# Performance work log

Measured on AMD Instinct MI355X. Metric: run time of the kernel, lower is better.

The kernel has to match this reference:

```python
import jax, jax.numpy as jnp
import numpy as np

N, H, E, C, V, K = 4096, 256, 128, 32, 64, 20


def setup_inputs() -> dict:
    key = jax.random.key(0)
    ks = jax.random.split(key, 16)
    f = lambda k, s: jax.random.normal(k, s, dtype=jnp.float32)
    return {
        "vec": f(ks[0], (N, H)),
        "inp": f(ks[1], (N, E)),
        "h_prev": f(ks[2], (N, H)),
        "c_prev": f(ks[3], (N, H)),
        "Wlin": f(ks[4], (C, V, H)) * 0.05,
        "blin": f(ks[5], (C, V)) * 0.05,
        "Wec": f(ks[6], (2, H)) * 0.05,
        "bec": f(ks[7], (2,)) * 0.05,
        "Wrel": f(ks[8], (5, H)) * 0.05,
        "brel": f(ks[9], (5,)) * 0.05,
        "W_ih": f(ks[10], (K, 4 * H, E)) * 0.05,
        "b_ih": f(ks[11], (K, 4 * H)) * 0.05,
        "W_hh": f(ks[12], (K, 4 * H, H)) * 0.05,
        "b_hh": f(ks[13], (K, 4 * H)) * 0.05,
        "category": jax.random.randint(ks[14], (N,), 0, C, dtype=jnp.int32),
        "cell_id": jax.random.randint(ks[15], (N,), 0, K, dtype=jnp.int32),
        "true_idx": jax.random.randint(jax.random.fold_in(key, 100), (N,), 0, V, dtype=jnp.int32),
        "ec_idx": jax.random.randint(jax.random.fold_in(key, 101), (N,), 0, 2, dtype=jnp.int32),
        "rel_idx": jax.random.randint(jax.random.fold_in(key, 102), (N,), 0, 5, dtype=jnp.int32),
    }


def _ce(logits, targets):
    # per-row cross entropy (same math as nn.CrossEntropyLoss per example)
    logp = jax.nn.log_softmax(logits, axis=-1)
    return -jnp.take_along_axis(logp, targets[:, None], axis=-1)[:, 0]


def reference(vec, inp, h_prev, c_prev, Wlin, blin, Wec, bec, Wrel, brel,
              W_ih, b_ih, W_hh, b_hh, category, cell_id, true_idx, ec_idx, rel_idx):
    # --- get_log_odds: per-category tiny linear head, selected by category ---
    logits_all = jnp.einsum('nh,cvh->ncv', vec, Wlin) + blin          # [N,C,V]
    logits = jnp.take_along_axis(logits_all, category[:, None, None].astype(jnp.int32), axis=1)[:, 0]  # [N,V]
    logits_ec = vec @ Wec.T + bec                                      # [N,2]
    logits_rel = vec @ Wrel.T + brel                                   # [N,5]

    # --- calculate_loss: CE over valid children + ec + rel ---
    losses = _ce(logits, true_idx) + _ce(logits_ec, ec_idx) + _ce(logits_rel, rel_idx)  # [N]

    # --- get_next: per-child-index LSTMCell, selected by cell_id ---
    gates_all = (jnp.einsum('ne,kge->nkg', inp, W_ih)
                 + jnp.einsum('nh,kgh->nkg', h_prev, W_hh)
                 + b_ih + b_hh)                                        # [N,K,4H]
    gates = jnp.take_along_axis(gates_all, cell_id[:, None, None].astype(jnp.int32), axis=1)[:, 0]  # [N,4H]
    i, f, g, o = jnp.split(gates, 4, axis=-1)                          # torch LSTMCell gate order i,f,g,o
    c_next = jax.nn.sigmoid(f) * c_prev + jax.nn.sigmoid(i) * jnp.tanh(g)
    h_next = jax.nn.sigmoid(o) * jnp.tanh(c_next)

    # pack: [N, 1 + 2H] = loss | h_next | c_next
    return jnp.concatenate([losses[:, None], h_next, c_next], axis=-1)
```

## Files before the change

kernel.cpp:

```cpp
#include <hip/hip_runtime.h>
#include <hip/hip_bf16.h>
#include <math.h>

#define Nn 4096
#define Hdim 256
#define Edim 128
#define Cdim 32
#define Vdim 64
#define Kdim 20
#define G4H 1024
#define OUTS 513

#define SK 512
#define SC 256
#define RK_OFF 64
#define RC_OFF (RK_OFF + Kdim * SK)
#define NLI 18496
#define NSI 18497
#define ITL 18498
#define ITS (ITL + 640)

#define LSTM_REGION 592
#define LOSS_REGION 320
#define GRID (LSTM_REGION + LOSS_REGION)

typedef short bf16x8 __attribute__((ext_vector_type(8)));
typedef float f32x4 __attribute__((ext_vector_type(4)));

__device__ __forceinline__ float sigmoidf_(float x) { return 1.0f / (1.0f + expf(-x)); }

__device__ __forceinline__ bf16x8 cvt8(float4 f0, float4 f1) {
    bf16x8 r;
    __hip_bfloat16 h;
    h = __float2bfloat16(f0.x); r[0] = *(short*)&h;
    h = __float2bfloat16(f0.y); r[1] = *(short*)&h;
    h = __float2bfloat16(f0.z); r[2] = *(short*)&h;
    h = __float2bfloat16(f0.w); r[3] = *(short*)&h;
    h = __float2bfloat16(f1.x); r[4] = *(short*)&h;
    h = __float2bfloat16(f1.y); r[5] = *(short*)&h;
    h = __float2bfloat16(f1.z); r[6] = *(short*)&h;
    h = __float2bfloat16(f1.w); r[7] = *(short*)&h;
    return r;
}

__device__ __forceinline__ void gl_lds16(const float* g, void* l) {
    __builtin_amdgcn_global_load_lds((const __attribute__((address_space(1))) void*)g,
                                     (__attribute__((address_space(3))) void*)l, 16, 0, 0);
}

__device__ __forceinline__ int swz(int r) { return ((r & 3) << 1) | ((r >> 2) & 1); }

__global__ __launch_bounds__(1024) void k_bucket(const int* __restrict__ cell_id,
                                                 const int* __restrict__ category,
                                                 int* __restrict__ ws) {
    __shared__ int cnt[32];
    __shared__ int off[33];
    int t = threadIdx.x;
    if (t < 32) cnt[t] = 0;
    __syncthreads();
    int i0 = t * 4;
    if (blockIdx.x == 0) {
        int4 v = ((const int4*)cell_id)[t];
        int r;
        r = atomicAdd(&cnt[v.x], 1); if (r < SK) ws[RK_OFF + v.x * SK + r] = i0 + 0;
        r = atomicAdd(&cnt[v.y], 1); if (r < SK) ws[RK_OFF + v.y * SK + r] = i0 + 1;
        r = atomicAdd(&cnt[v.z], 1); if (r < SK) ws[RK_OFF + v.z * SK + r] = i0 + 2;
        r = atomicAdd(&cnt[v.w], 1); if (r < SK) ws[RK_OFF + v.w * SK + r] = i0 + 3;
        __syncthreads();
        if (t == 0) {
            int a = 0;
            for (int kk = 0; kk < Kdim; kk++) { off[kk] = a; a += (min(cnt[kk], SK) + 31) >> 5; }
            ws[NLI] = a * 4;
        }
        __syncthreads();
        if (t < Kdim) {
            int ns = (min(cnt[t], SK) + 31) >> 5;
            int base = off[t];
            for (int s = 0; s < ns; s++)
                for (int hq = 0; hq < 4; hq++)
                    ws[ITL + (base + s) * 4 + hq] = t | (s << 8) | (hq << 16);
        }
        if (t < 32) ws[t] = min(cnt[t], SK);
    } else {
        int4 v = ((const int4*)category)[t];
        int r;
        r = atomicAdd(&cnt[v.x], 1); if (r < SC) ws[RC_OFF + v.x * SC + r] = i0 + 0;
        r = atomicAdd(&cnt[v.y], 1); if (r < SC) ws[RC_OFF + v.y * SC + r] = i0 + 1;
        r = atomicAdd(&cnt[v.z], 1); if (r < SC) ws[RC_OFF + v.z * SC + r] = i0 + 2;
        r = atomicAdd(&cnt[v.w], 1); if (r < SC) ws[RC_OFF + v.w * SC + r] = i0 + 3;
        __syncthreads();
        if (t == 0) {
            int a = 0;
            for (int cc = 0; cc < Cdim; cc++) { off[cc] = a; a += (min(cnt[cc], SC) + 15) >> 4; }
            ws[NSI] = a;
        }
        __syncthreads();
        if (t < Cdim) {
            int ns = (min(cnt[t], SC) + 15) >> 4;
            int base = off[t];
            for (int s = 0; s < ns; s++)
                ws[ITS + base + s] = t | (s << 8);
        }
        if (t < 32) ws[32 + t] = min(cnt[t], SC);
    }
}

__global__ __launch_bounds__(256, 4) void k_main(
    const float* __restrict__ vec, const float* __restrict__ inp,
    const float* __restrict__ h_prev, const float* __restrict__ c_prev,
    const float* __restrict__ Wlin, const float* __restrict__ blin,
    const float* __restrict__ Wec, const float* __restrict__ bec,
    const float* __restrict__ Wrel, const float* __restrict__ brel,
    const float* __restrict__ W_ih, const float* __restrict__ b_ih,
    const float* __restrict__ W_hh, const float* __restrict__ b_hh,
    const int* __restrict__ true_idx, const int* __restrict__ ec_idx, const int* __restrict__ rel_idx,
    const int* __restrict__ ws,
    float* __restrict__ out)
{
    __shared__ __align__(16) char smem[36864];

    int b = blockIdx.x, t = threadIdx.x;
    int w = t >> 6, l = t & 63;
    int l15 = l & 15, quad = l >> 4;
    int lrow8 = l >> 3, lslot = l & 7;
    int p0 = (quad * 2) ^ swz(l15);

    if (b < LSTM_REGION) {
        if (b >= ws[NLI]) return;
        int item = ws[ITL + b];
        int k = item & 255, s = (item >> 8) & 255, hq = item >> 16;
        int cntk = ws[k];
        int rcount = min(32, cntk - s * 32);
        int reg_row = ws[RK_OFF + k * SK + s * 32 + min(l & 31, rcount - 1)];

        float* Wb = (float*)smem;
        float* Xb = (float*)(smem + 32768);
        const float* Wih_k = W_ih + (size_t)k * G4H * Edim;
        const float* Whh_k = W_hh + (size_t)k * G4H * Hdim;

        int xr = w * 8 + lrow8;
        int xrow = __shfl(reg_row, xr);
        int xg = lslot ^ swz(xr);

        int h = hq * 64 + w * 16 + l15;
        float bs[4];
        #pragma unroll
        for (int g = 0; g < 4; g++)
            bs[g] = b_ih[(size_t)k * G4H + g * Hdim + h] + b_hh[(size_t)k * G4H + g * Hdim + h];
        float cp[2][4];
        #pragma unroll
        for (int m = 0; m < 2; m++)
            #pragma unroll
            for (int reg = 0; reg < 4; reg++) {
                int r = m * 16 + quad * 4 + reg;
                int row = __shfl(reg_row, r);
                cp[m][reg] = c_prev[(size_t)row * Hdim + h];
            }

        f32x4 acc[2][4];
        #pragma unroll
        for (int m = 0; m < 2; m++)
            #pragma unroll
            for (int g = 0; g < 4; g++)
                acc[m][g] = (f32x4){0.f, 0.f, 0.f, 0.f};

        for (int st = 0; st < 12; st++) {
            int k0 = st * 32;
            const float* Wsrc; int stride, ko;
            if (k0 < Edim) { Wsrc = Wih_k; stride = Edim; ko = k0; }
            else           { Wsrc = Whh_k; stride = Hdim; ko = k0 - Edim; }
            __syncthreads();
            #pragma unroll
            for (int j = 0; j < 8; j++) {
                int r = w * 64 + j * 8 + lrow8;
                int g = lslot ^ swz(r);
                int gate = r >> 6, hl = r & 63;
                gl_lds16(Wsrc + (size_t)(gate * Hdim + hq * 64 + hl) * stride + ko + g * 4,
                         Wb + (w * 64 + j * 8) * 32);
            }
            {
                const float* Xs = (k0 < Edim) ? inp + (size_t)xrow * Edim + ko
                                              : h_prev + (size_t)xrow * Hdim + ko;
                gl_lds16(Xs + xg * 4, Xb + (w * 8) * 32);
            }
            __syncthreads();

            bf16x8 af[2], bfr[4];
            #pragma unroll
            for (int m = 0; m < 2; m++) {
                int row = m * 16 + l15;
                float4 lo = *(float4*)(Xb + row * 32 + p0 * 4);
                float4 hi = *(float4*)(Xb + row * 32 + (p0 ^ 1) * 4);
                af[m] = cvt8(lo, hi);
            }
            #pragma unroll
            for (int g = 0; g < 4; g++) {
                int row = g * 64 + w * 16 + l15;
                float4 lo = *(float4*)(Wb + row * 32 + p0 * 4);
                float4 hi = *(float4*)(Wb + row * 32 + (p0 ^ 1) * 4);
                bfr[g] = cvt8(lo, hi);
            }
            #pragma unroll
            for (int m = 0; m < 2; m++)
                #pragma unroll
                for (int g = 0; g < 4; g++)
                    acc[m][g] = __builtin_amdgcn_mfma_f32_16x16x32_bf16(af[m], bfr[g], acc[m][g], 0, 0, 0);
        }

        #pragma unroll
        for (int m = 0; m < 2; m++) {
            #pragma unroll
            for (int reg = 0; reg < 4; reg++) {
                int r = m * 16 + quad * 4 + reg;
                int row = __shfl(reg_row, r);
                if (r < rcount) {
                    float iv = acc[m][0][reg] + bs[0];
                    float fv = acc[m][1][reg] + bs[1];
                    float gv = acc[m][2][reg] + bs[2];
                    float ov = acc[m][3][reg] + bs[3];
                    float cn = sigmoidf_(fv) * cp[m][reg] + sigmoidf_(iv) * tanhf(gv);
                    float hn = sigmoidf_(ov) * tanhf(cn);
                    out[(size_t)row * OUTS + 1 + h] = hn;
                    out[(size_t)row * OUTS + 1 + Hdim + h] = cn;
                }
            }
        }
    } else {
        int b2 = b - LSTM_REGION;
        if (b2 >= ws[NSI]) return;
        int item = ws[ITS + b2];
        int c = item & 255, s = item >> 8;
        int cntc = ws[32 + c];
        int rcount = min(16, cntc - s * 16);
        int reg_row = ws[RC_OFF + c * SC + s * 16 + min(l & 15, rcount - 1)];

        float* Wb = (float*)smem;
        float* Vb = (float*)(smem + 10240);
        float* Lg = (float*)(smem + 12288);

        int xr = (w >= 2) ? ((w - 2) * 8 + lrow8) : 0;
        int xrow = __shfl(reg_row, xr);
        int xg = lslot ^ swz(xr);

        f32x4 a0 = (f32x4){0.f, 0.f, 0.f, 0.f};
        f32x4 a1 = (f32x4){0.f, 0.f, 0.f, 0.f};

        for (int st = 0; st < 8; st++) {
            int ko = st * 32;
            __syncthreads();
            for (int n = w; n < 10; n += 4) {
                int r = n * 8 + lrow8;
                int g = lslot ^ swz(r);
                const float* srcW;
                if (r < 64)      srcW = Wlin + ((size_t)c * Vdim + r) * Hdim;
                else if (r < 66) srcW = Wec + (size_t)(r - 64) * Hdim;
                else if (r < 71) srcW = Wrel + (size_t)(r - 66) * Hdim;
                else             srcW = Wlin + (size_t)c * Vdim * Hdim;
                gl_lds16(srcW + ko + g * 4, Wb + n * 8 * 32);
            }
            if (w >= 2)
                gl_lds16(vec + (size_t)xrow * Hdim + ko + xg * 4, Vb + ((w - 2) * 8) * 32);
            __syncthreads();

            bf16x8 af;
            {
                float4 lo = *(float4*)(Vb + l15 * 32 + p0 * 4);
                float4 hi = *(float4*)(Vb + l15 * 32 + (p0 ^ 1) * 4);
                af = cvt8(lo, hi);
            }
            {
                int row = w * 16 + l15;
                float4 lo = *(float4*)(Wb + row * 32 + p0 * 4);
                float4 hi = *(float4*)(Wb + row * 32 + (p0 ^ 1) * 4);
                bf16x8 b0 = cvt8(lo, hi);
                a0 = __builtin_amdgcn_mfma_f32_16x16x32_bf16(af, b0, a0, 0, 0, 0);
            }
            if (w == 3) {
                int row = 64 + l15;
                float4 lo = *(float4*)(Wb + row * 32 + p0 * 4);
                float4 hi = *(float4*)(Wb + row * 32 + (p0 ^ 1) * 4);
                bf16x8 b1 = cvt8(lo, hi);
                a1 = __builtin_amdgcn_mfma_f32_16x16x32_bf16(af, b1, a1, 0, 0, 0);
            }
        }
        __syncthreads();
        {
            int col = w * 16 + l15;
            float bb = blin[c * Vdim + col];
            #pragma unroll
            for (int reg = 0; reg < 4; reg++)
                Lg[(quad * 4 + reg) * 84 + col] = a0[reg] + bb;
            if (w == 3) {
                int col1 = 64 + l15;
                float bb1 = (l15 < 2) ? bec[l15] : ((l15 < 7) ? brel[l15 - 2] : 0.f);
                #pragma unroll
                for (int reg = 0; reg < 4; reg++)
                    Lg[(quad * 4 + reg) * 84 + col1] = a1[reg] + bb1;
            }
        }
        __syncthreads();
        for (int rr = 0; rr < 4; rr++) {
            int r = w * 4 + rr;
            if (r >= rcount) break;
            int orig = __shfl(reg_row, r);
            float lg = Lg[r * 84 + l];
            float mx = lg;
            for (int ss = 32; ss >= 1; ss >>= 1) mx = fmaxf(mx, __shfl_xor(mx, ss));
            float sm = expf(lg - mx);
            for (int ss = 32; ss >= 1; ss >>= 1) sm += __shfl_xor(sm, ss);
            float lt = __shfl(lg, true_idx[orig]);
            float loss = mx + logf(sm) - lt;
            if (l == 0) {
                float l0 = Lg[r * 84 + 64], l1 = Lg[r * 84 + 65];
                float me2 = fmaxf(l0, l1);
                loss += me2 + logf(expf(l0 - me2) + expf(l1 - me2)) - ((ec_idx[orig] == 0) ? l0 : l1);
                float rl[5] = { Lg[r * 84 + 66], Lg[r * 84 + 67], Lg[r * 84 + 68], Lg[r * 84 + 69], Lg[r * 84 + 70] };
                float mr = rl[0];
                #pragma unroll
                for (int i = 1; i < 5; i++) mr = fmaxf(mr, rl[i]);
                float sr = 0.f;
                #pragma unroll
                for (int i = 0; i < 5; i++) sr += expf(rl[i] - mr);
                loss += mr + logf(sr) - rl[rel_idx[orig]];
                out[(size_t)orig * OUTS] = loss;
            }
        }
    }
}

extern "C" void kernel_launch(void* const* d_in, const int* in_sizes, int n_in,
                              void* d_out, int out_size, void* d_ws, size_t ws_size,
                              hipStream_t stream) {
    const float* vec      = (const float*)d_in[0];
    const float* inp      = (const float*)d_in[1];
    const float* h_prev   = (const float*)d_in[2];
    const float* c_prev   = (const float*)d_in[3];
    const float* Wlin     = (const float*)d_in[4];
    const float* blin     = (const float*)d_in[5];
    const float* Wec      = (const float*)d_in[6];
    const float* bec      = (const float*)d_in[7];
    const float* Wrel     = (const float*)d_in[8];
    const float* brel     = (const float*)d_in[9];
    const float* W_ih     = (const float*)d_in[10];
    const float* b_ih     = (const float*)d_in[11];
    const float* W_hh     = (const float*)d_in[12];
    const float* b_hh     = (const float*)d_in[13];
    const int*   category = (const int*)d_in[14];
    const int*   cell_id  = (const int*)d_in[15];
    const int*   true_idx = (const int*)d_in[16];
    const int*   ec_idx   = (const int*)d_in[17];
    const int*   rel_idx  = (const int*)d_in[18];
    float* out = (float*)d_out;
    int* ws = (int*)d_ws;

    k_bucket<<<2, 1024, 0, stream>>>(cell_id, category, ws);
    k_main<<<GRID, 256, 0, stream>>>(
        vec, inp, h_prev, c_prev, Wlin, blin, Wec, bec, Wrel, brel,
        W_ih, b_ih, W_hh, b_hh, true_idx, ec_idx, rel_idx, ws, out);
}
```

Measured before the change: 140.4 us.

## Pre-convert LSTM weights to bf16 fragment layout in a separate kernel

After: 150.7 us. 1.07x slower.

```diff
diff --git a/kernel.cpp b/kernel.cpp
--- a/kernel.cpp
+++ b/kernel.cpp
@@ -20,12 +20,16 @@
 #define ITL 18498
 #define ITS (ITL + 640)
 
+#define OFF_WF 81920
+#define NWF (Kdim * 4 * 12)
+
 #define LSTM_REGION 592
 #define LOSS_REGION 320
 #define GRID (LSTM_REGION + LOSS_REGION)
 
 typedef short bf16x8 __attribute__((ext_vector_type(8)));
 typedef float f32x4 __attribute__((ext_vector_type(4)));
+typedef unsigned short u16;
 
 __device__ __forceinline__ float sigmoidf_(float x) { return 1.0f / (1.0f + expf(-x)); }
 
@@ -43,7 +47,7 @@
     return r;
 }
 
-__device__ __forceinline__ void gl_lds16(const float* g, void* l) {
+__device__ __forceinline__ void gl_lds16(const void* g, void* l) {
     __builtin_amdgcn_global_load_lds((const __attribute__((address_space(1))) void*)g,
                                      (__attribute__((address_space(3))) void*)l, 16, 0, 0);
 }
@@ -105,19 +109,43 @@
     }
 }
 
+__global__ __launch_bounds__(256) void k_wconv(
+    const float* __restrict__ W_ih, const float* __restrict__ W_hh,
+    int* __restrict__ ws)
+{
+    u16* WF = (u16*)((char*)ws + OFF_WF);
+    int b = blockIdx.x, t = threadIdx.x;
+    int l = t & 63, sub = t >> 6;
+    int c16 = l & 15, qd = l >> 4;
+
+    int k = b / 48; int r = b - k * 48; int hq = r / 12; int st = r - hq * 12;
+    int kk = st * 32 + qd * 8;
+    #pragma unroll
+    for (int rep = 0; rep < 4; rep++) {
+        int idx = sub * 4 + rep;
+        int g = idx >> 2, wv = idx & 3;
+        int row = g * Hdim + hq * 64 + wv * 16 + c16;
+        const float* p = (st < 4)
+            ? (W_ih + ((size_t)k * G4H + row) * Edim + kk)
+            : (W_hh + ((size_t)k * G4H + row) * Hdim + (kk - Edim));
+        float4 lo = *(const float4*)p;
+        float4 hi = *(const float4*)(p + 4);
+        *(bf16x8*)(WF + ((size_t)(((k * 4 + hq) * 12 + st) * 16 + idx) * 64 + l) * 8) = cvt8(lo, hi);
+    }
+}
+
 __global__ __launch_bounds__(256, 4) void k_main(
     const float* __restrict__ vec, const float* __restrict__ inp,
     const float* __restrict__ h_prev, const float* __restrict__ c_prev,
     const float* __restrict__ Wlin, const float* __restrict__ blin,
     const float* __restrict__ Wec, const float* __restrict__ bec,
     const float* __restrict__ Wrel, const float* __restrict__ brel,
-    const float* __restrict__ W_ih, const float* __restrict__ b_ih,
-    const float* __restrict__ W_hh, const float* __restrict__ b_hh,
+    const float* __restrict__ b_ih, const float* __restrict__ b_hh,
     const int* __restrict__ true_idx, const int* __restrict__ ec_idx, const int* __restrict__ rel_idx,
     const int* __restrict__ ws,
     float* __restrict__ out)
 {
-    __shared__ __align__(16) char smem[36864];
+    __shared__ __align__(16) char smem[40960];
 
     int b = blockIdx.x, t = threadIdx.x;
     int w = t >> 6, l = t & 63;
@@ -133,14 +161,15 @@
         int rcount = min(32, cntk - s * 32);
         int reg_row = ws[RK_OFF + k * SK + s * 32 + min(l & 31, rcount - 1)];
 
-        float* Wb = (float*)smem;
+        char* Wb = smem;
         float* Xb = (float*)(smem + 32768);
-        const float* Wih_k = W_ih + (size_t)k * G4H * Edim;
-        const float* Whh_k = W_hh + (size_t)k * G4H * Hdim;
+        const char* WFbase = (const char*)ws + OFF_WF + (size_t)((k * 4 + hq) * 12) * 16384;
 
         int xr = w * 8 + lrow8;
         int xrow = __shfl(reg_row, xr);
         int xg = lslot ^ swz(xr);
+        const float* xinp = inp + (size_t)xrow * Edim;
+        const float* xhp  = h_prev + (size_t)xrow * Hdim;
 
         int h = hq * 64 + w * 16 + l15;
         float bs[4];
@@ -164,47 +193,41 @@
             for (int g = 0; g < 4; g++)
                 acc[m][g] = (f32x4){0.f, 0.f, 0.f, 0.f};
 
-        for (int st = 0; st < 12; st++) {
-            int k0 = st * 32;
-            const float* Wsrc; int stride, ko;
-            if (k0 < Edim) { Wsrc = Wih_k; stride = Edim; ko = k0; }
-            else           { Wsrc = Whh_k; stride = Hdim; ko = k0 - Edim; }
+        for (int st = 0; st < 6; st++) {
             __syncthreads();
+            const char* WFp = WFbase + (size_t)(st * 2) * 16384;
             #pragma unroll
             for (int j = 0; j < 8; j++) {
-                int r = w * 64 + j * 8 + lrow8;
-                int g = lslot ^ swz(r);
-                int gate = r >> 6, hl = r & 63;
-                gl_lds16(Wsrc + (size_t)(gate * Hdim + hq * 64 + hl) * stride + ko + g * 4,
-                         Wb + (w * 64 + j * 8) * 32);
-            }
-            {
-                const float* Xs = (k0 < Edim) ? inp + (size_t)xrow * Edim + ko
-                                              : h_prev + (size_t)xrow * Hdim + ko;
-                gl_lds16(Xs + xg * 4, Xb + (w * 8) * 32);
+                int grp = j * 4 + w;
+                gl_lds16(WFp + grp * 1024 + l * 16, Wb + grp * 1024);
+            }
+            #pragma unroll
+            for (int half = 0; half < 2; half++) {
+                int k0 = (st * 2 + half) * 32;
+                const float* Xs = (k0 < Edim) ? xinp + k0 : xhp + (k0 - Edim);
+                gl_lds16(Xs + xg * 4, Xb + half * 1024 + (w * 8) * 32);
             }
             __syncthreads();
 
-            bf16x8 af[2], bfr[4];
-            #pragma unroll
-            for (int m = 0; m < 2; m++) {
-                int row = m * 16 + l15;
-                float4 lo = *(float4*)(Xb + row * 32 + p0 * 4);
-                float4 hi = *(float4*)(Xb + row * 32 + (p0 ^ 1) * 4);
-                af[m] = cvt8(lo, hi);
-            }
-            #pragma unroll
-            for (int g = 0; g < 4; g++) {
-                int row = g * 64 + w * 16 + l15;
-                float4 lo = *(float4*)(Wb + row * 32 + p0 * 4);
-                float4 hi = *(float4*)(Wb + row * 32 + (p0 ^ 1) * 4);
-                bfr[g] = cvt8(lo, hi);
-            }
-            #pragma unroll
-            for (int m = 0; m < 2; m++)
+            #pragma unroll
+            for (int kk = 0; kk < 2; kk++) {
+                bf16x8 af[2], bfr[4];
+                #pragma unroll
+                for (int m = 0; m < 2; m++) {
+                    int row = m * 16 + l15;
+                    float4 lo = *(float4*)(Xb + kk * 1024 + row * 32 + p0 * 4);
+                    float4 hi = *(float4*)(Xb + kk * 1024 + row * 32 + (p0 ^ 1) * 4);
+                    af[m] = cvt8(lo, hi);
+                }
                 #pragma unroll
                 for (int g = 0; g < 4; g++)
-                    acc[m][g] = __builtin_amdgcn_mfma_f32_16x16x32_bf16(af[m], bfr[g], acc[m][g], 0, 0, 0);
+                    bfr[g] = *(bf16x8*)(Wb + kk * 16384 + (g * 4 + w) * 1024 + l * 16);
+                #pragma unroll
+                for (int m = 0; m < 2; m++)
+                    #pragma unroll
+                    for (int g = 0; g < 4; g++)
+                        acc[m][g] = __builtin_amdgcn_mfma_f32_16x16x32_bf16(af[m], bfr[g], acc[m][g], 0, 0, 0);
+            }
         }
 
         #pragma unroll
@@ -354,7 +377,8 @@
     int* ws = (int*)d_ws;
 
     k_bucket<<<2, 1024, 0, stream>>>(cell_id, category, ws);
+    k_wconv<<<NWF, 256, 0, stream>>>(W_ih, W_hh, ws);
     k_main<<<GRID, 256, 0, stream>>>(
         vec, inp, h_prev, c_prev, Wlin, blin, Wec, bec, Wrel, brel,
-        W_ih, b_ih, W_hh, b_hh, true_idx, ec_idx, rel_idx, ws, out);
-}
+        b_ih, b_hh, true_idx, ec_idx, rel_idx, ws, out);
+}
```
